# Performance work log

Measured on AMD Instinct MI355X. Metric: run time of the kernel, lower is better.

## Reference

```python
import jax, jax.numpy as jnp
import numpy as np

B, T, D, H = 4, 2048, 1024, 16
HD = D // H  # 64
NEG = -np.finfo(np.float32).max


def setup_inputs() -> dict:
    key = jax.random.key(0)
    ks = jax.random.split(key, 9)
    s = 1.0 / np.sqrt(D)
    return {
        "x": jax.random.normal(ks[0], (B, T, D), jnp.float32),
        "wq": jax.random.normal(ks[1], (D, D), jnp.float32) * s,
        "bq": jax.random.normal(ks[2], (D,), jnp.float32) * 0.02,
        "wk": jax.random.normal(ks[3], (D, D), jnp.float32) * s,
        "bk": jax.random.normal(ks[4], (D,), jnp.float32) * 0.02,
        "wv": jax.random.normal(ks[5], (D, D), jnp.float32) * s,
        "bv": jax.random.normal(ks[6], (D,), jnp.float32) * 0.02,
        "wo": jax.random.normal(ks[7], (D, D), jnp.float32) * s,
        "bo": jax.random.normal(ks[8], (D,), jnp.float32) * 0.02,
    }


def reference(x, wq, bq, wk, bk, wv, bv, wo, bo):
    b, t, d = x.shape
    # separate Q, K, V projections, reshape to (B, H, T, HD)
    def proj(w, bias):
        y = x @ w + bias
        return y.reshape(b, t, H, HD).transpose(0, 2, 1, 3)
    q = proj(wq, bq)
    k = proj(wk, bk)
    v = proj(wv, bv)
    scale = 1.0 / np.sqrt(HD).astype(np.float32)
    scores = jnp.einsum("bhqd,bhkd->bhqk", q, k) * scale  # (B,H,T,T)
    # causal mask: -max_float on strictly upper triangle (matches source)
    mask = jnp.triu(jnp.full((t, t), NEG, jnp.float32), k=1)
    attn = jax.nn.softmax(scores + mask, axis=-1)
    out = jnp.einsum("bhqk,bhkd->bhqd", attn, v)
    out = out.transpose(0, 2, 1, 3).reshape(b, t, d)
    return out @ wo + bo
```

## Files before the change

### kernel.cpp

```cpp
#include <hip/hip_runtime.h>

typedef __bf16 bf16x8 __attribute__((ext_vector_type(8)));
typedef float f32x4 __attribute__((ext_vector_type(4)));

#define B_ 4
#define T_ 2048
#define D_ 1024
#define H_ 16
#define HD_ 64
#define M_ 8192
#define QSCALE 0.1803368801111204f

__device__ __forceinline__ ushort f2b(float f) {
  union { float f; unsigned u; } v; v.f = f;
  unsigned u = v.u;
  return (ushort)((u + 0x7FFFu + ((u >> 16) & 1u)) >> 16);
}

__device__ __forceinline__ unsigned pkbf(float a, float b) {
  union { float f; unsigned u; } va, vb; va.f = a; vb.f = b;
  return __builtin_amdgcn_perm(vb.u + 0x8000u, va.u + 0x8000u, 0x07060302u);
}

__global__ __launch_bounds__(256) void cast_x_kernel(const float* __restrict__ x,
                                                     ushort* __restrict__ xb) {
  int idx = blockIdx.x * 256 + threadIdx.x;
  float4 v = ((const float4*)x)[idx];
  ushort4 o;
  o.x = f2b(v.x); o.y = f2b(v.y); o.z = f2b(v.z); o.w = f2b(v.w);
  ((ushort4*)xb)[idx] = o;
}

__global__ __launch_bounds__(256) void transpose_w_kernel(
    const float* __restrict__ wq, const float* __restrict__ wk,
    const float* __restrict__ wv, const float* __restrict__ wo,
    ushort* __restrict__ wt_qkv, ushort* __restrict__ wt_o) {
  __shared__ float tile[32][33];
  int z = blockIdx.z;
  const float* src = (z == 0) ? wq : (z == 1) ? wk : (z == 2) ? wv : wo;
  ushort* dst = (z < 3) ? (wt_qkv + (size_t)z * D_ * D_) : wt_o;
  int n0 = blockIdx.x * 32, k0 = blockIdx.y * 32;
  int tx = threadIdx.x & 31, ty = threadIdx.x >> 5;
  for (int i = 0; i < 4; i++) {
    int r = ty + i * 8;
    tile[r][tx] = src[(size_t)(k0 + r) * D_ + n0 + tx];
  }
  __syncthreads();
  for (int i = 0; i < 4; i++) {
    int r = ty + i * 8;
    dst[(size_t)(n0 + r) * D_ + k0 + tx] = f2b(tile[tx][r]);
  }
}

__global__ __launch_bounds__(256) void gemm_kernel(
    const ushort* __restrict__ A, const ushort* __restrict__ Bt, int mode,
    const float* __restrict__ bias_q, const float* __restrict__ bias_k,
    const float* __restrict__ bias_v,
    ushort* __restrict__ qb, ushort* __restrict__ kb, ushort* __restrict__ vtb,
    float* __restrict__ outf) {
  __shared__ ushort As[128][72];
  __shared__ ushort Bs[128][72];
  int tid = threadIdx.x;
  int wave = tid >> 6, lane = tid & 63, lrow = lane >> 4, lcol = lane & 15;
  int m0 = blockIdx.y * 128, n0 = blockIdx.x * 128;
  int wm = (wave & 1) * 64, wn = (wave >> 1) * 64;

  f32x4 zero = {0.f, 0.f, 0.f, 0.f};
  f32x4 acc[4][4];
  for (int i = 0; i < 4; i++)
    for (int j = 0; j < 4; j++) acc[i][j] = zero;

  for (int k0 = 0; k0 < D_; k0 += 64) {
    for (int i = 0; i < 4; i++) {
      int c = i * 256 + tid;
      int r = c >> 3, col = (c & 7) * 8;
      *(uint4*)&As[r][col] = *(const uint4*)&A[(size_t)(m0 + r) * D_ + k0 + col];
      *(uint4*)&Bs[r][col] = *(const uint4*)&Bt[(size_t)(n0 + r) * D_ + k0 + col];
    }
    __syncthreads();
    for (int ks = 0; ks < 2; ks++) {
      bf16x8 af[4], bf[4];
      for (int mt = 0; mt < 4; mt++)
        af[mt] = *(const bf16x8*)&As[wm + mt * 16 + lcol][ks * 32 + lrow * 8];
      for (int nt = 0; nt < 4; nt++)
        bf[nt] = *(const bf16x8*)&Bs[wn + nt * 16 + lcol][ks * 32 + lrow * 8];
      for (int mt = 0; mt < 4; mt++)
        for (int nt = 0; nt < 4; nt++)
          acc[mt][nt] = __builtin_amdgcn_mfma_f32_16x16x32_bf16(
              af[mt], bf[nt], acc[mt][nt], 0, 0, 0);
    }
    __syncthreads();
  }

  if (mode == 0) {
    int proj = n0 >> 10;
    const float* bias = (proj == 0) ? bias_q : (proj == 1) ? bias_k : bias_v;
    for (int mt = 0; mt < 4; mt++) {
      int gm0 = m0 + wm + mt * 16 + lrow * 4;
      int b = gm0 >> 11, tp = gm0 & 2047;
      for (int nt = 0; nt < 4; nt++) {
        int gn = n0 + wn + nt * 16 + lcol;
        int inner = gn & 1023;
        int h = inner >> 6, hd = inner & 63;
        float bv = bias[inner];
        if (proj == 0) {
          size_t base = ((size_t)(b * H_ + h) * T_ + tp) * HD_ + hd;
          for (int r = 0; r < 4; r++)
            qb[base + (size_t)r * HD_] = f2b((acc[mt][nt][r] + bv) * QSCALE);
        } else if (proj == 1) {
          size_t base = ((size_t)(b * H_ + h) * T_ + tp) * HD_ + hd;
          for (int r = 0; r < 4; r++)
            kb[base + (size_t)r * HD_] = f2b(acc[mt][nt][r] + bv);
        } else {
          ushort4 pk;
          pk.x = f2b(acc[mt][nt][0] + bv);
          pk.y = f2b(acc[mt][nt][1] + bv);
          pk.z = f2b(acc[mt][nt][2] + bv);
          pk.w = f2b(acc[mt][nt][3] + bv);
          *(ushort4*)&vtb[((size_t)(b * H_ + h) * HD_ + hd) * T_ + tp] = pk;
        }
      }
    }
  } else {
    for (int mt = 0; mt < 4; mt++) {
      int gm0 = m0 + wm + mt * 16 + lrow * 4;
      for (int nt = 0; nt < 4; nt++) {
        int gn = n0 + wn + nt * 16 + lcol;
        float bv = bias_q[gn];
        for (int r = 0; r < 4; r++)
          outf[(size_t)(gm0 + r) * D_ + gn] = acc[mt][nt][r] + bv;
      }
    }
  }
}

__global__ __launch_bounds__(256) void flash_kernel(
    const ushort* __restrict__ qb, const ushort* __restrict__ kb,
    const ushort* __restrict__ vtb, ushort* __restrict__ ob) {
  __shared__ ushort Ks[64][80];
  __shared__ ushort Vs[64][80];
  __shared__ ushort Ps[4][16][80];
  int tid = threadIdx.x;
  int wave = tid >> 6, lane = tid & 63, lrow = lane >> 4, lcol = lane & 15;
  int p = blockIdx.x;
  int bh = blockIdx.y;
  int b = bh >> 4, h = bh & 15;
  const ushort* qh = qb + (size_t)bh * T_ * HD_;
  const ushort* kh = kb + (size_t)bh * T_ * HD_;
  const ushort* vh = vtb + (size_t)bh * HD_ * T_;

  int r0 = tid >> 3, cb0 = (tid & 7) * 8;
  uint4 kr0 = *(const uint4*)&kh[(size_t)r0 * HD_ + cb0];
  uint4 kr1 = *(const uint4*)&kh[(size_t)(r0 + 32) * HD_ + cb0];
  uint4 vr0 = *(const uint4*)&vh[(size_t)r0 * T_ + cb0];
  uint4 vr1 = *(const uint4*)&vh[(size_t)(r0 + 32) * T_ + cb0];

  f32x4 zero = {0.f, 0.f, 0.f, 0.f};

  for (int pass = 0; pass < 2; pass++) {
    int qtile = pass ? p : (31 - p);
    int q0w = qtile * 64 + wave * 16;
    bf16x8 qf[2];
    for (int ks = 0; ks < 2; ks++)
      qf[ks] = *(const bf16x8*)&qh[(size_t)(q0w + lcol) * HD_ + ks * 32 + lrow * 8];

    float m_run = -1e30f, l_run = 0.f;
    f32x4 accO[4];
    for (int mt = 0; mt < 4; mt++) accO[mt] = zero;

    for (int j = 0; j <= qtile; j++) {
      __syncthreads();
      *(uint4*)&Ks[r0][cb0] = kr0;
      *(uint4*)&Ks[r0 + 32][cb0] = kr1;
      *(uint4*)&Vs[r0][cb0] = vr0;
      *(uint4*)&Vs[r0 + 32][cb0] = vr1;
      __syncthreads();

      if (j < qtile || pass == 0) {
        int jn = (j < qtile) ? j + 1 : 0;
        kr0 = *(const uint4*)&kh[(size_t)(jn * 64 + r0) * HD_ + cb0];
        kr1 = *(const uint4*)&kh[(size_t)(jn * 64 + r0 + 32) * HD_ + cb0];
        vr0 = *(const uint4*)&vh[(size_t)r0 * T_ + jn * 64 + cb0];
        vr1 = *(const uint4*)&vh[(size_t)(r0 + 32) * T_ + jn * 64 + cb0];
      }

      f32x4 st[4];
      for (int mt = 0; mt < 4; mt++) st[mt] = zero;
      for (int ks = 0; ks < 2; ks++)
        for (int mt = 0; mt < 4; mt++) {
          bf16x8 kf = *(const bf16x8*)&Ks[mt * 16 + lcol][ks * 32 + lrow * 8];
          st[mt] = __builtin_amdgcn_mfma_f32_16x16x32_bf16(kf, qf[ks], st[mt], 0, 0, 0);
        }

      if (j == qtile) {
        int q_g = q0w + lcol;
        for (int mt = 0; mt < 4; mt++)
          for (int r = 0; r < 4; r++) {
            int kv_g = j * 64 + mt * 16 + lrow * 4 + r;
            if (kv_g > q_g) st[mt][r] = -1e30f;
          }
      }

      float mx = fmaxf(
          fmaxf(fmaxf(fmaxf(st[0][0], st[0][1]), fmaxf(st[0][2], st[0][3])),
                fmaxf(fmaxf(st[1][0], st[1][1]), fmaxf(st[1][2], st[1][3]))),
          fmaxf(fmaxf(fmaxf(st[2][0], st[2][1]), fmaxf(st[2][2], st[2][3])),
                fmaxf(fmaxf(st[3][0], st[3][1]), fmaxf(st[3][2], st[3][3]))));
      mx = fmaxf(mx, __shfl_xor(mx, 16));
      mx = fmaxf(mx, __shfl_xor(mx, 32));
      float mn = fmaxf(m_run, mx);
      float alpha = __builtin_amdgcn_exp2f(m_run - mn);
      m_run = mn;
      float rs = 0.f;
      for (int mt = 0; mt < 4; mt++)
        for (int r = 0; r < 4; r++) {
          float pv = __builtin_amdgcn_exp2f(st[mt][r] - mn);
          st[mt][r] = pv;
          rs += pv;
        }
      rs += __shfl_xor(rs, 16);
      rs += __shfl_xor(rs, 32);
      l_run = l_run * alpha + rs;

      for (int mt = 0; mt < 4; mt++) {
        uint2 pk;
        pk.x = pkbf(st[mt][0], st[mt][1]);
        pk.y = pkbf(st[mt][2], st[mt][3]);
        *(uint2*)&Ps[wave][lcol][mt * 16 + lrow * 4] = pk;
      }

      for (int mt = 0; mt < 4; mt++)
        for (int r = 0; r < 4; r++) accO[mt][r] *= alpha;

      for (int ks = 0; ks < 2; ks++) {
        bf16x8 pf = *(const bf16x8*)&Ps[wave][lcol][ks * 32 + lrow * 8];
        for (int mt = 0; mt < 4; mt++) {
          bf16x8 vf = *(const bf16x8*)&Vs[mt * 16 + lcol][ks * 32 + lrow * 8];
          accO[mt] = __builtin_amdgcn_mfma_f32_16x16x32_bf16(vf, pf, accO[mt], 0, 0, 0);
        }
      }
    }

    float linv = 1.f / l_run;
    int t = q0w + lcol;
    size_t base = ((size_t)b * T_ + t) * D_ + h * HD_;
    for (int mt = 0; mt < 4; mt++) {
      uint2 pk;
      pk.x = pkbf(accO[mt][0] * linv, accO[mt][1] * linv);
      pk.y = pkbf(accO[mt][2] * linv, accO[mt][3] * linv);
      *(uint2*)&ob[base + mt * 16 + lrow * 4] = pk;
    }
  }
}

extern "C" void kernel_launch(void* const* d_in, const int* in_sizes, int n_in,
                              void* d_out, int out_size, void* d_ws, size_t ws_size,
                              hipStream_t stream) {
  (void)in_sizes; (void)n_in; (void)out_size; (void)ws_size;
  const float* x  = (const float*)d_in[0];
  const float* wq = (const float*)d_in[1];
  const float* bq = (const float*)d_in[2];
  const float* wk = (const float*)d_in[3];
  const float* bk = (const float*)d_in[4];
  const float* wv = (const float*)d_in[5];
  const float* bv = (const float*)d_in[6];
  const float* wo = (const float*)d_in[7];
  const float* bo = (const float*)d_in[8];
  float* out = (float*)d_out;

  char* ws = (char*)d_ws;
  ushort* xb     = (ushort*)(ws);
  ushort* wt_qkv = (ushort*)(ws + 16777216);
  ushort* wt_o   = (ushort*)(ws + 23068672);
  ushort* qb     = (ushort*)(ws + 25165824);
  ushort* kb     = (ushort*)(ws + 41943040);
  ushort* vtb    = (ushort*)(ws + 58720256);
  ushort* ob     = (ushort*)(ws + 75497472);

  cast_x_kernel<<<8192, 256, 0, stream>>>(x, xb);
  transpose_w_kernel<<<dim3(32, 32, 4), 256, 0, stream>>>(wq, wk, wv, wo, wt_qkv, wt_o);
  gemm_kernel<<<dim3(24, 64), 256, 0, stream>>>(xb, wt_qkv, 0, bq, bk, bv, qb, kb, vtb, nullptr);
  flash_kernel<<<dim3(16, 64), 256, 0, stream>>>(qb, kb, vtb, ob);
  gemm_kernel<<<dim3(8, 64), 256, 0, stream>>>(ob, wt_o, 1, bo, nullptr, nullptr,
                                               nullptr, nullptr, nullptr, out);
}
```

Baseline: 288.6 us.

## Double-buffer GEMM LDS tiles with register prefetch and XOR swizzle

Restructures the projection GEMM main loop to prefetch the next K-tile from global memory into registers while MFMAs run on the current LDS buffer, then stores it to a second LDS buffer. This halves the barriers per iteration and hides global load latency. It also replaces the padded LDS layout with an XOR-swizzled unpadded layout to avoid bank conflicts. The cost is doubled LDS use and more live registers, which may reduce occupancy.

```diff
diff --git a/kernel.cpp b/kernel.cpp
--- a/kernel.cpp
+++ b/kernel.cpp
@@ -58,38 +58,82 @@
     const float* __restrict__ bias_v,
     ushort* __restrict__ qb, ushort* __restrict__ kb, ushort* __restrict__ vtb,
     float* __restrict__ outf) {
-  __shared__ ushort As[128][72];
-  __shared__ ushort Bs[128][72];
+  __shared__ ushort As[2][128][64];
+  __shared__ ushort Bs[2][128][64];
   int tid = threadIdx.x;
   int wave = tid >> 6, lane = tid & 63, lrow = lane >> 4, lcol = lane & 15;
   int m0 = blockIdx.y * 128, n0 = blockIdx.x * 128;
   int wm = (wave & 1) * 64, wn = (wave >> 1) * 64;
 
+  int rb = tid >> 3;
+  int dc = tid & 7;
+  int scv = dc ^ (rb & 7);
+  const ushort* aBase = A + (size_t)(m0 + rb) * D_ + scv * 8;
+  const ushort* bBase = Bt + (size_t)(n0 + rb) * D_ + scv * 8;
+
   f32x4 zero = {0.f, 0.f, 0.f, 0.f};
   f32x4 acc[4][4];
   for (int i = 0; i < 4; i++)
     for (int j = 0; j < 4; j++) acc[i][j] = zero;
 
+  int swz = lcol & 7;
+
+  {
+    uint4 a0 = *(const uint4*)(aBase);
+    uint4 a1 = *(const uint4*)(aBase + (size_t)32 * D_);
+    uint4 a2 = *(const uint4*)(aBase + (size_t)64 * D_);
+    uint4 a3 = *(const uint4*)(aBase + (size_t)96 * D_);
+    uint4 b0 = *(const uint4*)(bBase);
+    uint4 b1 = *(const uint4*)(bBase + (size_t)32 * D_);
+    uint4 b2 = *(const uint4*)(bBase + (size_t)64 * D_);
+    uint4 b3 = *(const uint4*)(bBase + (size_t)96 * D_);
+    *(uint4*)&As[0][rb][dc * 8] = a0;
+    *(uint4*)&As[0][rb + 32][dc * 8] = a1;
+    *(uint4*)&As[0][rb + 64][dc * 8] = a2;
+    *(uint4*)&As[0][rb + 96][dc * 8] = a3;
+    *(uint4*)&Bs[0][rb][dc * 8] = b0;
+    *(uint4*)&Bs[0][rb + 32][dc * 8] = b1;
+    *(uint4*)&Bs[0][rb + 64][dc * 8] = b2;
+    *(uint4*)&Bs[0][rb + 96][dc * 8] = b3;
+  }
+
   for (int k0 = 0; k0 < D_; k0 += 64) {
-    for (int i = 0; i < 4; i++) {
-      int c = i * 256 + tid;
-      int r = c >> 3, col = (c & 7) * 8;
-      *(uint4*)&As[r][col] = *(const uint4*)&A[(size_t)(m0 + r) * D_ + k0 + col];
-      *(uint4*)&Bs[r][col] = *(const uint4*)&Bt[(size_t)(n0 + r) * D_ + k0 + col];
-    }
+    int cur = (k0 >> 6) & 1, nxt = cur ^ 1;
+    int kn = (k0 + 64 < D_) ? k0 + 64 : k0;
     __syncthreads();
+
+    uint4 a0 = *(const uint4*)(aBase + kn);
+    uint4 a1 = *(const uint4*)(aBase + (size_t)32 * D_ + kn);
+    uint4 a2 = *(const uint4*)(aBase + (size_t)64 * D_ + kn);
+    uint4 a3 = *(const uint4*)(aBase + (size_t)96 * D_ + kn);
+    uint4 b0 = *(const uint4*)(bBase + kn);
+    uint4 b1 = *(const uint4*)(bBase + (size_t)32 * D_ + kn);
+    uint4 b2 = *(const uint4*)(bBase + (size_t)64 * D_ + kn);
+    uint4 b3 = *(const uint4*)(bBase + (size_t)96 * D_ + kn);
+
     for (int ks = 0; ks < 2; ks++) {
       bf16x8 af[4], bf[4];
+      int ch = ((ks * 4 + lrow) ^ swz) * 8;
       for (int mt = 0; mt < 4; mt++)
-        af[mt] = *(const bf16x8*)&As[wm + mt * 16 + lcol][ks * 32 + lrow * 8];
+        af[mt] = *(const bf16x8*)&As[cur][wm + mt * 16 + lcol][ch];
       for (int nt = 0; nt < 4; nt++)
-        bf[nt] = *(const bf16x8*)&Bs[wn + nt * 16 + lcol][ks * 32 + lrow * 8];
+        bf[nt] = *(const bf16x8*)&Bs[cur][wn + nt * 16 + lcol][ch];
       for (int mt = 0; mt < 4; mt++)
         for (int nt = 0; nt < 4; nt++)
           acc[mt][nt] = __builtin_amdgcn_mfma_f32_16x16x32_bf16(
               af[mt], bf[nt], acc[mt][nt], 0, 0, 0);
     }
-    __syncthreads();
+
+    if (k0 + 64 < D_) {
+      *(uint4*)&As[nxt][rb][dc * 8] = a0;
+      *(uint4*)&As[nxt][rb + 32][dc * 8] = a1;
+      *(uint4*)&As[nxt][rb + 64][dc * 8] = a2;
+      *(uint4*)&As[nxt][rb + 96][dc * 8] = a3;
+      *(uint4*)&Bs[nxt][rb][dc * 8] = b0;
+      *(uint4*)&Bs[nxt][rb + 32][dc * 8] = b1;
+      *(uint4*)&Bs[nxt][rb + 64][dc * 8] = b2;
+      *(uint4*)&Bs[nxt][rb + 96][dc * 8] = b3;
+    }
   }
 
   if (mode == 0) {
```

After: 280.0 us. 3.0% less time.
